# Optimization experiments

Hardware: AMD Instinct MI355X
Metric: run time of the kernel (lower is better)

## Reference

```python
import jax, jax.numpy as jnp
import numpy as np

TAU = 0.01  # softmax temperature used throughout the module


def _cross_en(sim_matrix):
    # -mean(diag(log_softmax(sim, -1)))
    logpt = jax.nn.log_softmax(sim_matrix, axis=-1)
    return -jnp.mean(jnp.diagonal(logpt))


def setup_inputs() -> dict:
    key = jax.random.key(0)
    k1, k2, k3, k4 = jax.random.split(key, 4)
    bs, nw, nf, d = 128, 80, 64, 768
    inp = {
        "traj_output": jax.random.normal(k1, (bs, d), dtype=jnp.float32),
        "frame_features": jax.random.normal(k2, (bs, nf, d), dtype=jnp.float32),
        "sentence_output": jax.random.normal(k3, (bs, d), dtype=jnp.float32),
        "word_features": jax.random.normal(k4, (bs, nw, d), dtype=jnp.float32),
        # nn.Parameter(torch.eye(...)) -- init_weights does not touch these
        "global_mat_weight": jnp.eye(d, dtype=jnp.float32),
        "word_logit_weight": jnp.eye(nw, dtype=jnp.float32),
        "frame_logit_weight": jnp.eye(nf, dtype=jnp.float32),
        "local_mat_weight": jnp.eye(d, dtype=jnp.float32),
        "frame_mat_weight": jnp.eye(nf, dtype=jnp.float32),
        "word_mat_weight": jnp.eye(nw, dtype=jnp.float32),
        "frame_mat_weight2": jnp.eye(nf, dtype=jnp.float32),
        "word_mat_weight2": jnp.eye(nw, dtype=jnp.float32),
    }
    return inp


def reference(traj_output, frame_features, sentence_output, word_features,
              global_mat_weight, word_logit_weight, frame_logit_weight,
              local_mat_weight, frame_mat_weight, word_mat_weight,
              frame_mat_weight2, word_mat_weight2):
    # traj_output: [bs,d]; frame_features: [bs,nf,d]; sentence_output: [bs,d]; word_features: [bs,nw,d]

    # --- traj_sent: (sent @ G) @ traj^T -> [bs_t, bs_v] ---
    traj_sent_sim = (sentence_output @ global_mat_weight) @ traj_output.T

    # --- video_word: word_features @ traj^T -> [bs_t, nw, bs_v] ---
    A = jnp.einsum('twd,vd->twv', word_features, traj_output)
    sA = jax.nn.softmax(A / TAU, axis=1)
    # (softmax.permute(0,2,1) @ W).permute(0,2,1): contract nw axis with W
    wA = jnp.einsum('twv,wu->tuv', sA, word_logit_weight)
    video_word_sim = jnp.sum(A * wA, axis=1)  # [bs_t, bs_v]

    # --- sentence_frame: sent x frame -> [bs_v, bs_t, nf] (torch broadcast batching) ---
    B = jnp.einsum('td,vfd->vtf', sentence_output, frame_features)
    sB = jax.nn.softmax(B / TAU, axis=-1)
    sentence_frame_sim = jnp.sum(B * (sB @ frame_logit_weight), axis=-1).T  # [bs_t, bs_v]

    # --- frame_word: fine-grained sim [bs_t, nw, bs_v, nf] ---
    S = jnp.einsum('twd,vfd->twvf', word_features @ local_mat_weight, frame_features)
    # word-level logit: softmax over nw, mix with word_mat_weight, weighted sum over nw
    sw = jax.nn.softmax(S / TAU, axis=1)
    word_level = jnp.sum(jnp.einsum('twvf,wu->tuvf', sw, word_mat_weight) * S, axis=1)  # [t,v,f]
    # frame-level logit: softmax over nf, mix with frame_mat_weight, weighted sum over nf
    sf = jax.nn.softmax(S / TAU, axis=-1)
    frame_level = jnp.sum((sf @ frame_mat_weight) * S, axis=-1)  # [t,w,v]
    # sent2frame: reduce nf of word_level
    smw = jax.nn.softmax(word_level / TAU, axis=-1)
    sent2frame = jnp.sum((smw @ frame_mat_weight2) * word_level, axis=-1)  # [t,v]
    # video2word: reduce nw of frame_level
    smf = jax.nn.softmax(frame_level / TAU, axis=1)
    video2word = jnp.sum(jnp.einsum('twv,wu->tuv', smf, word_mat_weight2) * frame_level, axis=1)  # [t,v]
    frame_word_sim = (sent2frame + video2word) / 2.0

    sim_matrix = (traj_sent_sim + video_word_sim + sentence_frame_sim + frame_word_sim) / 4.0

    sim_loss = (_cross_en(sim_matrix) + _cross_en(sim_matrix.T)) / 2.0
    return sim_loss
```

## Files before the change

### kernel.cpp

```cpp
#include <hip/hip_runtime.h>
#include <math.h>

#define BS 128
#define NW 80
#define NF 64
#define DD 768
#define INV_TAU 100.0f

typedef unsigned short u16;
typedef unsigned int u32;
typedef __attribute__((ext_vector_type(8))) short bf16x8;
typedef __attribute__((ext_vector_type(4))) float f32x4;

__device__ __forceinline__ u16 f2bf(float x) {
    unsigned b = __float_as_uint(x);
    return (u16)((b + 0x7fffu + ((b >> 16) & 1u)) >> 16);
}
__device__ __forceinline__ float bf2f(u16 h) { return __uint_as_float(((unsigned)h) << 16); }

__device__ __forceinline__ void gload_lds16(const void* gsrc, void* ldst) {
    __builtin_amdgcn_global_load_lds(
        (const __attribute__((address_space(1))) unsigned int*)gsrc,
        (__attribute__((address_space(3))) unsigned int*)ldst, 16, 0, 0);
}

__global__ __launch_bounds__(256) void k_sent_global(
    const float* __restrict__ sent, const float* __restrict__ G, float* __restrict__ sg)
{
    int idx = blockIdx.x * 256 + threadIdx.x;
    int t = idx / DD, e = idx % DD;
    const float* srow = sent + t * DD;
    float acc = 0.f;
    #pragma unroll 4
    for (int d = 0; d < DD; ++d) acc += srow[d] * G[d * DD + e];
    sg[idx] = acc;
}

__global__ __launch_bounds__(256) void k_traj_sent(
    const float* __restrict__ sg, const float* __restrict__ traj, float* __restrict__ sim)
{
    __shared__ float ss[16][33], tt[16][33];
    int tx = threadIdx.x & 15, ty = threadIdx.x >> 4;
    int t0 = blockIdx.y * 16, v0 = blockIdx.x * 16;
    float acc = 0.f;
    for (int kk = 0; kk < DD; kk += 32) {
        for (int l = threadIdx.x; l < 16 * 32; l += 256) {
            int r = l >> 5, c = l & 31;
            ss[r][c] = sg[(t0 + r) * DD + kk + c];
            tt[r][c] = traj[(v0 + r) * DD + kk + c];
        }
        __syncthreads();
        #pragma unroll
        for (int k = 0; k < 32; ++k) acc += ss[ty][k] * tt[tx][k];
        __syncthreads();
    }
    sim[(t0 + ty) * BS + v0 + tx] = 0.25f * acc;
}

__global__ __launch_bounds__(256) void k_prepw(
    const float* __restrict__ Wm, const float* __restrict__ Fm,
    u16* __restrict__ WmT_hi, u16* __restrict__ WmT_lo,
    u16* __restrict__ FmT_hi, u16* __restrict__ FmT_lo)
{
    int gid = blockIdx.x * 256 + threadIdx.x;
    if (gid < 80 * 96) {
        int u = gid / 96, w = gid % 96;
        float x = (w < 80) ? Wm[w * 80 + u] : 0.f;
        u16 h = f2bf(x);
        WmT_hi[gid] = h; WmT_lo[gid] = f2bf(x - bf2f(h));
    } else if (gid < 80 * 96 + 64 * 64) {
        int j = gid - 80 * 96;
        int fp = j >> 6, f = j & 63;
        float x = Fm[f * 64 + fp];
        u16 h = f2bf(x);
        FmT_hi[j] = h; FmT_lo[j] = f2bf(x - bf2f(h));
    }
}

__global__ __launch_bounds__(256) void k_ffsplit(
    const float* __restrict__ x, u16* __restrict__ hi, u16* __restrict__ lo)
{
    int i = blockIdx.x * 256 + threadIdx.x;
    float4 f = *(const float4*)&x[(size_t)i * 4];
    ushort4 h, l;
    h.x = f2bf(f.x); l.x = f2bf(f.x - bf2f(h.x));
    h.y = f2bf(f.y); l.y = f2bf(f.y - bf2f(h.y));
    h.z = f2bf(f.z); l.z = f2bf(f.z - bf2f(h.z));
    h.w = f2bf(f.w); l.w = f2bf(f.w - bf2f(h.w));
    *(ushort4*)&hi[(size_t)i * 4] = h;
    *(ushort4*)&lo[(size_t)i * 4] = l;
}

__global__ __launch_bounds__(256, 2) void k_wl(
    const float* __restrict__ wf, const float* __restrict__ L,
    u16* __restrict__ wl_hi, u16* __restrict__ wl_lo)
{
    __shared__ u16 Ah[128][72], Al[128][72];
    __shared__ u16 Bh[128][72], Bl[128][72];
    const int tid = threadIdx.x;
    const int lane = tid & 63, wid = tid >> 6;
    const int m0 = blockIdx.y * 128, n0 = blockIdx.x * 128;

    f32x4 acc[2][8];
    #pragma unroll
    for (int i = 0; i < 2; ++i)
        #pragma unroll
        for (int j = 0; j < 8; ++j) acc[i][j] = (f32x4){0.f, 0.f, 0.f, 0.f};

    for (int kk = 0; kk < DD; kk += 64) {
        #pragma unroll
        for (int p = 0; p < 8; ++p) {
            int row = p * 16 + (tid >> 4), c4 = tid & 15;
            float4 v = *(const float4*)&wf[(size_t)(m0 + row) * DD + kk + c4 * 4];
            ushort4 h, l;
            h.x = f2bf(v.x); l.x = f2bf(v.x - bf2f(h.x));
            h.y = f2bf(v.y); l.y = f2bf(v.y - bf2f(h.y));
            h.z = f2bf(v.z); l.z = f2bf(v.z - bf2f(h.z));
            h.w = f2bf(v.w); l.w = f2bf(v.w - bf2f(h.w));
            *(ushort4*)&Ah[row][c4 * 4] = h;
            *(ushort4*)&Al[row][c4 * 4] = l;
        }
        #pragma unroll
        for (int p = 0; p < 8; ++p) {
            int kr = p * 8 + (tid >> 5), c4 = tid & 31;
            float4 v = *(const float4*)&L[(size_t)(kk + kr) * DD + n0 + c4 * 4];
            #pragma unroll
            for (int jj = 0; jj < 4; ++jj) {
                int n = c4 * 4 + jj;
                float x = (jj == 0) ? v.x : (jj == 1) ? v.y : (jj == 2) ? v.z : v.w;
                u16 h = f2bf(x);
                int ka = kr ^ ((n & 7) << 3);
                Bh[n][ka] = h;
                Bl[n][ka] = f2bf(x - bf2f(h));
            }
        }
        __syncthreads();
        #pragma unroll
        for (int ks = 0; ks < 2; ++ks) {
            int koff = ks * 32 + (lane >> 4) * 8;
            bf16x8 ah[2], al[2];
            #pragma unroll
            for (int i = 0; i < 2; ++i) {
                int row = wid * 32 + 16 * i + (lane & 15);
                ah[i] = *(const bf16x8*)&Ah[row][koff];
                al[i] = *(const bf16x8*)&Al[row][koff];
            }
            #pragma unroll
            for (int j = 0; j < 8; ++j) {
                int n = 16 * j + (lane & 15);
                int kb = koff ^ ((n & 7) << 3);
                bf16x8 bh = *(const bf16x8*)&Bh[n][kb];
                bf16x8 bl = *(const bf16x8*)&Bl[n][kb];
                #pragma unroll
                for (int i = 0; i < 2; ++i) {
                    acc[i][j] = __builtin_amdgcn_mfma_f32_16x16x32_bf16(ah[i], bh, acc[i][j], 0, 0, 0);
                    acc[i][j] = __builtin_amdgcn_mfma_f32_16x16x32_bf16(ah[i], bl, acc[i][j], 0, 0, 0);
                    acc[i][j] = __builtin_amdgcn_mfma_f32_16x16x32_bf16(al[i], bh, acc[i][j], 0, 0, 0);
                }
            }
        }
        __syncthreads();
    }
    #pragma unroll
    for (int i = 0; i < 2; ++i)
        #pragma unroll
        for (int j = 0; j < 8; ++j)
            #pragma unroll
            for (int r = 0; r < 4; ++r) {
                float x = acc[i][j][r];
                int row = m0 + wid * 32 + 16 * i + ((lane >> 4) << 2) + r;
                int col = n0 + 16 * j + (lane & 15);
                size_t idx = (size_t)row * DD + col;
                u16 h = f2bf(x);
                wl_hi[idx] = h;
                wl_lo[idx] = f2bf(x - bf2f(h));
            }
}

__global__ __launch_bounds__(256, 2) void k_video_word(
    const float* __restrict__ wf, const float* __restrict__ traj,
    const float* __restrict__ Wl, float* __restrict__ sim)
{
    __shared__ __align__(16) float As[NW][36];
    __shared__ __align__(16) float Bs[64][36];
    __shared__ float Am[NW][65];
    __shared__ float Pm[NW][65];
    int tx = threadIdx.x & 15, ty = threadIdx.x >> 4;
    int t = blockIdx.y, v0 = blockIdx.x * 64;
    const float* wft = wf + t * NW * DD;
    float acc[5][4] = {};
    for (int kk = 0; kk < DD; kk += 32) {
        for (int l = threadIdx.x; l < NW * 32; l += 256) {
            int w = l >> 5, k = l & 31;
            As[w][k] = wft[w * DD + kk + k];
        }
        for (int l = threadIdx.x; l < 64 * 32; l += 256) {
            int v = l >> 5, k = l & 31;
            Bs[v][k] = traj[(v0 + v) * DD + kk + k];
        }
        __syncthreads();
        #pragma unroll
        for (int k = 0; k < 32; k += 4) {
            float4 a[5], b[4];
            #pragma unroll
            for (int i = 0; i < 5; ++i) a[i] = *(const float4*)&As[tx + 16 * i][k];
            #pragma unroll
            for (int j = 0; j < 4; ++j) b[j] = *(const float4*)&Bs[ty + 16 * j][k];
            #pragma unroll
            for (int i = 0; i < 5; ++i)
                #pragma unroll
                for (int j = 0; j < 4; ++j)
                    acc[i][j] += a[i].x * b[j].x + a[i].y * b[j].y + a[i].z * b[j].z + a[i].w * b[j].w;
        }
        __syncthreads();
    }
    #pragma unroll
    for (int i = 0; i < 5; ++i)
        #pragma unroll
        for (int j = 0; j < 4; ++j) Am[tx + 16 * i][ty + 16 * j] = acc[i][j];
    __syncthreads();
    if (threadIdx.x < 64) {
        int v = threadIdx.x;
        float m = -1e30f;
        for (int w = 0; w < NW; ++w) m = fmaxf(m, Am[w][v]);
        float s = 0.f;
        for (int w = 0; w < NW; ++w) { float e = __expf((Am[w][v] - m) * INV_TAU); Pm[w][v] = e; s += e; }
        float r = 1.f / s;
        for (int w = 0; w < NW; ++w) Pm[w][v] *= r;
    }
    __syncthreads();
    float mm[5][4] = {};
    for (int w = 0; w < NW; ++w) {
        float a[5], b[4];
        #pragma unroll
        for (int i = 0; i < 5; ++i) a[i] = Wl[w * NW + tx + 16 * i];
        #pragma unroll
        for (int j = 0; j < 4; ++j) b[j] = Pm[w][ty + 16 * j];
        #pragma unroll
        for (int i = 0; i < 5; ++i)
            #pragma unroll
            for (int j = 0; j < 4; ++j) mm[i][j] += a[i] * b[j];
    }
    #pragma unroll
    for (int j = 0; j < 4; ++j) {
        float p = 0.f;
        #pragma unroll
        for (int i = 0; i < 5; ++i) p += mm[i][j] * Am[tx + 16 * i][ty + 16 * j];
        for (int o = 8; o; o >>= 1) p += __shfl_xor(p, o, 16);
        if (tx == 0) sim[t * BS + v0 + ty + 16 * j] += 0.25f * p;
    }
}

__global__ __launch_bounds__(256, 2) void k_sent_frame(
    const float* __restrict__ sent, const float* __restrict__ ff,
    const float* __restrict__ Fl, float* __restrict__ sim)
{
    __shared__ __align__(16) float Ss[64][36];
    __shared__ __align__(16) float Fs[64][36];
    __shared__ float Bm[64][65];
    __shared__ float Pm[64][65];
    int tx = threadIdx.x & 15, ty = threadIdx.x >> 4;
    int v = blockIdx.y, t0 = blockIdx.x * 64;
    const float* ffv = ff + v * NF * DD;
    float acc[4][4] = {};
    for (int kk = 0; kk < DD; kk += 32) {
        for (int l = threadIdx.x; l < 64 * 32; l += 256) {
            int r = l >> 5, k = l & 31;
            Ss[r][k] = sent[(t0 + r) * DD + kk + k];
            Fs[r][k] = ffv[r * DD + kk + k];
        }
        __syncthreads();
        #pragma unroll
        for (int k = 0; k < 32; k += 4) {
            float4 a[4], b[4];
            #pragma unroll
            for (int i = 0; i < 4; ++i) a[i] = *(const float4*)&Ss[tx + 16 * i][k];
            #pragma unroll
            for (int j = 0; j < 4; ++j) b[j] = *(const float4*)&Fs[ty + 16 * j][k];
            #pragma unroll
            for (int i = 0; i < 4; ++i)
                #pragma unroll
                for (int j = 0; j < 4; ++j)
                    acc[i][j] += a[i].x * b[j].x + a[i].y * b[j].y + a[i].z * b[j].z + a[i].w * b[j].w;
        }
        __syncthreads();
    }
    #pragma unroll
    for (int i = 0; i < 4; ++i)
        #pragma unroll
        for (int j = 0; j < 4; ++j) Bm[tx + 16 * i][ty + 16 * j] = acc[i][j];
    __syncthreads();
    if (threadIdx.x < 64) {
        int r = threadIdx.x;
        float m = -1e30f;
        for (int f = 0; f < NF; ++f) m = fmaxf(m, Bm[r][f]);
        float s = 0.f;
        for (int f = 0; f < NF; ++f) { float e = __expf((Bm[r][f] - m) * INV_TAU); Pm[r][f] = e; s += e; }
        float rr = 1.f / s;
        for (int f = 0; f < NF; ++f) Pm[r][f] *= rr;
    }
    __syncthreads();
    float nn[4][4] = {};
    for (int f = 0; f < NF; ++f) {
        float a[4], b[4];
        #pragma unroll
        for (int i = 0; i < 4; ++i) a[i] = Pm[ty + 16 * i][f];
        #pragma unroll
        for (int j = 0; j < 4; ++j) b[j] = Fl[f * NF + tx + 16 * j];
        #pragma unroll
        for (int i = 0; i < 4; ++i)
            #pragma unroll
            for (int j = 0; j < 4; ++j) nn[i][j] += a[i] * b[j];
    }
    #pragma unroll
    for (int i = 0; i < 4; ++i) {
        float p = 0.f;
        #pragma unroll
        for (int j = 0; j < 4; ++j) p += nn[i][j] * Bm[ty + 16 * i][tx + 16 * j];
        for (int o = 8; o; o >>= 1) p += __shfl_xor(p, o, 16);
        if (tx == 0) sim[(t0 + ty + 16 * i) * BS + v] += 0.25f * p;
    }
}

__global__ __launch_bounds__(256, 3) void k_frame_word(
    const u16* __restrict__ wl_hi, const u16* __restrict__ wl_lo,
    const u16* __restrict__ ff_hi, const u16* __restrict__ ff_lo,
    const u16* __restrict__ WmT_hi, const u16* __restrict__ WmT_lo,
    const u16* __restrict__ FmT_hi, const u16* __restrict__ FmT_lo,
    const float* __restrict__ F2, const float* __restrict__ Wm2,
    float* __restrict__ sim)
{
    __shared__ __align__(16) union SH {
        u16 stage[18432];
        struct Post {
            float Sm[80][65];
            union PU {
                struct { u16 Pt_hi[64][104]; u16 Pt_lo[64][104]; } m1;
                struct { u16 P2_hi[80][72];  u16 P2_lo[80][72];  } m2;
            } u;
            float redm[4][64], reds[4][64];
            float wlv[64], flv[80], flvp[4][80];
            float smw[64], smf[80];
            float s2f, v2w;
        } post;
    } sh;

    const int tid = threadIdx.x;
    const int lane = tid & 63, wid = tid >> 6;
    const int col = lane & 15, grp = lane >> 4;
    const int v = blockIdx.x, t = blockIdx.y;

    f32x4 acc[5];
    #pragma unroll
    for (int i = 0; i < 5; ++i) acc[i] = (f32x4){0.f, 0.f, 0.f, 0.f};

    const int r8 = lane >> 3, s8 = lane & 7;
    const int gk = s8 ^ r8;

    for (int kk = 0; kk < DD; kk += 64) {
        for (int seg = wid; seg < 36; seg += 4) {
            const u16* src;
            int ldsoff;
            if (seg < 10) {
                int g = seg, row = g * 8 + r8;
                src = wl_hi + (size_t)(t * NW + row) * DD + kk + gk * 8;
                ldsoff = g * 512;
            } else if (seg < 20) {
                int g = seg - 10, row = g * 8 + r8;
                src = wl_lo + (size_t)(t * NW + row) * DD + kk + gk * 8;
                ldsoff = 5120 + g * 512;
            } else if (seg < 28) {
                int g = seg - 20, row = g * 8 + r8;
                src = ff_hi + (size_t)(v * NF + row) * DD + kk + gk * 8;
                ldsoff = 10240 + g * 512;
            } else {
                int g = seg - 28, row = g * 8 + r8;
                src = ff_lo + (size_t)(v * NF + row) * DD + kk + gk * 8;
                ldsoff = 14336 + g * 512;
            }
            gload_lds16(src, (void*)&sh.stage[ldsoff]);
        }
        __syncthreads();
        const u16* st = sh.stage;
        #pragma unroll
        for (int ks = 0; ks < 2; ++ks) {
            const int sl = (ks << 2) + grp;
            bf16x8 afh[5], afl[5], bfh, bfl;
            #pragma unroll
            for (int i = 0; i < 5; ++i) {
                int row = col + 16 * i;
                int off = row * 64 + ((sl ^ (row & 7)) << 3);
                afh[i] = *(const bf16x8*)&st[off];
                afl[i] = *(const bf16x8*)&st[5120 + off];
            }
            {
                int row = col + 16 * wid;
                int off = row * 64 + ((sl ^ (row & 7)) << 3);
                bfh = *(const bf16x8*)&st[10240 + off];
                bfl = *(const bf16x8*)&st[14336 + off];
            }
            #pragma unroll
            for (int i = 0; i < 5; ++i) {
                acc[i] = __builtin_amdgcn_mfma_f32_16x16x32_bf16(afh[i], bfh, acc[i], 0, 0, 0);
                acc[i] = __builtin_amdgcn_mfma_f32_16x16x32_bf16(afh[i], bfl, acc[i], 0, 0, 0);
                acc[i] = __builtin_amdgcn_mfma_f32_16x16x32_bf16(afl[i], bfh, acc[i], 0, 0, 0);
            }
        }
        __syncthreads();
    }

    #pragma unroll
    for (int i = 0; i < 5; ++i)
        #pragma unroll
        for (int r = 0; r < 4; ++r)
            sh.post.Sm[16 * i + (grp << 2) + r][col + (wid << 4)] = acc[i][r];
    __syncthreads();

    {
        const int f = tid & 63, q = tid >> 6, w0 = q * 20;
        float m = -1e30f;
        for (int w = w0; w < w0 + 20; ++w) m = fmaxf(m, sh.post.Sm[w][f]);
        float s = 0.f;
        for (int w = w0; w < w0 + 20; ++w) s += __expf((sh.post.Sm[w][f] - m) * INV_TAU);
        sh.post.redm[q][f] = m; sh.post.reds[q][f] = s;
        __syncthreads();
        float M = -1e30f;
        #pragma unroll
        for (int qq = 0; qq < 4; ++qq) M = fmaxf(M, sh.post.redm[qq][f]);
        float Dn = 0.f;
        #pragma unroll
        for (int qq = 0; qq < 4; ++qq) Dn += sh.post.reds[qq][f] * __expf((sh.post.redm[qq][f] - M) * INV_TAU);
        float rDn = 1.f / Dn;
        #pragma unroll
        for (int mp = 0; mp < 10; ++mp) {
            int w = w0 + 2 * mp;
            float e0 = __expf((sh.post.Sm[w][f] - M) * INV_TAU) * rDn;
            float e1 = __expf((sh.post.Sm[w + 1][f] - M) * INV_TAU) * rDn;
            u16 h0 = f2bf(e0), h1 = f2bf(e1);
            u16 l0 = f2bf(e0 - bf2f(h0)), l1 = f2bf(e1 - bf2f(h1));
            *(u32*)&sh.post.u.m1.Pt_hi[f][w] = (u32)h0 | ((u32)h1 << 16);
            *(u32*)&sh.post.u.m1.Pt_lo[f][w] = (u32)l0 | ((u32)l1 << 16);
        }
        if (tid < 64) {
            uint4 z = {0, 0, 0, 0};
            *(uint4*)&sh.post.u.m1.Pt_hi[tid][80] = z;
            *(uint4*)&sh.post.u.m1.Pt_hi[tid][88] = z;
            *(uint4*)&sh.post.u.m1.Pt_lo[tid][80] = z;
            *(uint4*)&sh.post.u.m1.Pt_lo[tid][88] = z;
        }
    }
    __syncthreads();

    {
        f32x4 d1[5];
        #pragma unroll
        for (int i = 0; i < 5; ++i) d1[i] = (f32x4){0.f, 0.f, 0.f, 0.f};
        #pragma unroll
        for (int ks = 0; ks < 3; ++ks) {
            int baddr = (wid * 16 + col) * 104 + ks * 32 + grp * 8;
            bf16x8 bh = *(const bf16x8*)&sh.post.u.m1.Pt_hi[0][baddr];
            bf16x8 bl = *(const bf16x8*)&sh.post.u.m1.Pt_lo[0][baddr];
            #pragma unroll
            for (int i = 0; i < 5; ++i) {
                int aaddr = (16 * i + col) * 96 + ks * 32 + grp * 8;
                bf16x8 ah = *(const bf16x8*)&WmT_hi[aaddr];
                bf16x8 al = *(const bf16x8*)&WmT_lo[aaddr];
                d1[i] = __builtin_amdgcn_mfma_f32_16x16x32_bf16(ah, bh, d1[i], 0, 0, 0);
                d1[i] = __builtin_amdgcn_mfma_f32_16x16x32_bf16(ah, bl, d1[i], 0, 0, 0);
                d1[i] = __builtin_amdgcn_mfma_f32_16x16x32_bf16(al, bh, d1[i], 0, 0, 0);
            }
        }
        float p = 0.f;
        #pragma unroll
        for (int i = 0; i < 5; ++i)
            #pragma unroll
            for (int r = 0; r < 4; ++r)
                p += d1[i][r] * sh.post.Sm[16 * i + (grp << 2) + r][wid * 16 + col];
        p += __shfl_xor(p, 16);
        p += __shfl_xor(p, 32);
        if (lane < 16) sh.post.wlv[wid * 16 + lane] = p;
    }
    __syncthreads();

    if (tid < 160) {
        const int w = tid >> 1, h = tid & 1, f0 = h * 32;
        float m = -1e30f;
        for (int c = 0; c < 32; ++c) m = fmaxf(m, sh.post.Sm[w][f0 + c]);
        m = fmaxf(m, __shfl_xor(m, 1));
        float s = 0.f;
        for (int c = 0; c < 32; ++c) s += __expf((sh.post.Sm[w][f0 + c] - m) * INV_TAU);
        s += __shfl_xor(s, 1);
        float r = 1.f / s;
        #pragma unroll
        for (int mp = 0; mp < 16; ++mp) {
            int f = f0 + 2 * mp;
            float e0 = __expf((sh.post.Sm[w][f] - m) * INV_TAU) * r;
            float e1 = __expf((sh.post.Sm[w][f + 1] - m) * INV_TAU) * r;
            u16 h0 = f2bf(e0), h1 = f2bf(e1);
            u16 l0 = f2bf(e0 - bf2f(h0)), l1 = f2bf(e1 - bf2f(h1));
            *(u32*)&sh.post.u.m2.P2_hi[w][f] = (u32)h0 | ((u32)h1 << 16);
            *(u32*)&sh.post.u.m2.P2_lo[w][f] = (u32)l0 | ((u32)l1 << 16);
        }
    }
    __syncthreads();

    {
        f32x4 d2[5];
        #pragma unroll
        for (int i = 0; i < 5; ++i) d2[i] = (f32x4){0.f, 0.f, 0.f, 0.f};
        #pragma unroll
        for (int ks = 0; ks < 2; ++ks) {
            int baddr = (wid * 16 + col) * 64 + ks * 32 + grp * 8;
            bf16x8 bh = *(const bf16x8*)&FmT_hi[baddr];
            bf16x8 bl = *(const bf16x8*)&FmT_lo[baddr];
            #pragma unroll
            for (int i = 0; i < 5; ++i) {
                int aaddr = (16 * i + col) * 72 + ks * 32 + grp * 8;
                bf16x8 ah = *(const bf16x8*)&sh.post.u.m2.P2_hi[0][aaddr];
                bf16x8 al = *(const bf16x8*)&sh.post.u.m2.P2_lo[0][aaddr];
                d2[i] = __builtin_amdgcn_mfma_f32_16x16x32_bf16(ah, bh, d2[i], 0, 0, 0);
                d2[i] = __builtin_amdgcn_mfma_f32_16x16x32_bf16(ah, bl, d2[i], 0, 0, 0);
                d2[i] = __builtin_amdgcn_mfma_f32_16x16x32_bf16(al, bh, d2[i], 0, 0, 0);
            }
        }
        #pragma unroll
        for (int i = 0; i < 5; ++i)
            #pragma unroll
            for (int r = 0; r < 4; ++r) {
                int w = 16 * i + (grp << 2) + r;
                float p = d2[i][r] * sh.post.Sm[w][wid * 16 + col];
                p += __shfl_xor(p, 1);
                p += __shfl_xor(p, 2);
                p += __shfl_xor(p, 4);
                p += __shfl_xor(p, 8);
                if (col == 0) sh.post.flvp[wid][w] = p;
            }
    }
    __syncthreads();
    if (tid < 80)
        sh.post.flv[tid] = sh.post.flvp[0][tid] + sh.post.flvp[1][tid]
                         + sh.post.flvp[2][tid] + sh.post.flvp[3][tid];
    __syncthreads();

    if (wid == 0) {
        float x = sh.post.wlv[lane];
        float m = x;
        #pragma unroll
        for (int o = 32; o; o >>= 1) m = fmaxf(m, __shfl_xor(m, o));
        float e = __expf((x - m) * INV_TAU);
        float s = e;
        #pragma unroll
        for (int o = 32; o; o >>= 1) s += __shfl_xor(s, o);
        sh.post.smw[lane] = e / s;
    } else if (wid == 1) {
        float x0 = sh.post.flv[lane];
        float x1 = (lane < 16) ? sh.post.flv[64 + lane] : -1e30f;
        float m = fmaxf(x0, x1);
        #pragma unroll
        for (int o = 32; o; o >>= 1) m = fmaxf(m, __shfl_xor(m, o));
        float e0 = __expf((x0 - m) * INV_TAU);
        float e1 = (lane < 16) ? __expf((x1 - m) * INV_TAU) : 0.f;
        float s = e0 + e1;
        #pragma unroll
        for (int o = 32; o; o >>= 1) s += __shfl_xor(s, o);
        sh.post.smf[lane] = e0 / s;
        if (lane < 16) sh.post.smf[64 + lane] = e1 / s;
    }
    __syncthreads();

    if (wid == 0) {
        float g = 0.f;
        for (int f = 0; f < NF; ++f) g += sh.post.smw[f] * F2[f * NF + lane];
        float p = g * sh.post.wlv[lane];
        #pragma unroll
        for (int o = 32; o; o >>= 1) p += __shfl_xor(p, o);
        if (lane == 0) sh.post.s2f = p;
    } else if (wid == 1) {
        float g = 0.f;
        for (int w = 0; w < NW; ++w) g += sh.post.smf[w] * Wm2[w * NW + lane];
        float p = g * sh.post.flv[lane];
        if (lane < 16) {
            float g2 = 0.f;
            for (int w = 0; w < NW; ++w) g2 += sh.post.smf[w] * Wm2[w * NW + 64 + lane];
            p += g2 * sh.post.flv[64 + lane];
        }
        #pragma unroll
        for (int o = 32; o; o >>= 1) p += __shfl_xor(p, o);
        if (lane == 0) sh.post.v2w = p;
    }
    __syncthreads();
    if (tid == 0) sim[t * BS + v] += 0.125f * (sh.post.s2f + sh.post.v2w);
}

__global__ __launch_bounds__(256) void k_loss(const float* __restrict__ sim, float* __restrict__ out)
{
    __shared__ float S[BS][BS + 1];
    __shared__ float lr[BS], lc[BS];
    for (int l = threadIdx.x; l < BS * BS; l += 256) {
        int r = l >> 7, c = l & 127;
        S[r][c] = sim[l];
    }
    __syncthreads();
    int tid = threadIdx.x;
    if (tid < BS) {
        float m = -1e30f;
        for (int c = 0; c < BS; ++c) m = fmaxf(m, S[tid][c]);
        float s = 0.f;
        for (int c = 0; c < BS; ++c) s += __expf(S[tid][c] - m);
        lr[tid] = m + __logf(s);
    } else {
        int c = tid - BS;
        float m = -1e30f;
        for (int r = 0; r < BS; ++r) m = fmaxf(m, S[r][c]);
        float s = 0.f;
        for (int r = 0; r < BS; ++r) s += __expf(S[r][c] - m);
        lc[c] = m + __logf(s);
    }
    __syncthreads();
    if (tid == 0) {
        float a = 0.f;
        for (int i = 0; i < BS; ++i) a += S[i][i] - 0.5f * lr[i] - 0.5f * lc[i];
        out[0] = -a / (float)BS;
    }
}

extern "C" void kernel_launch(void* const* d_in, const int* in_sizes, int n_in,
                              void* d_out, int out_size, void* d_ws, size_t ws_size,
                              hipStream_t stream)
{
    const float* traj = (const float*)d_in[0];
    const float* ff   = (const float*)d_in[1];
    const float* sent = (const float*)d_in[2];
    const float* wf   = (const float*)d_in[3];
    const float* G    = (const float*)d_in[4];
    const float* Wl   = (const float*)d_in[5];
    const float* Fl   = (const float*)d_in[6];
    const float* L    = (const float*)d_in[7];
    const float* Fm   = (const float*)d_in[8];
    const float* Wm   = (const float*)d_in[9];
    const float* F2   = (const float*)d_in[10];
    const float* Wm2  = (const float*)d_in[11];
    float* out = (float*)d_out;
    char* base = (char*)d_ws;

    float* sg     = (float*)(base);
    float* sim    = (float*)(base + 393216);
    u16*   wl_hi  = (u16*)(base + 458752);
    u16*   wl_lo  = (u16*)(base + 16187392);
    u16*   ff_hi  = (u16*)(base + 31916032);
    u16*   ff_lo  = (u16*)(base + 44498944);
    u16*   WmT_hi = (u16*)(base + 57081856);
    u16*   WmT_lo = (u16*)(base + 57097216);
    u16*   FmT_hi = (u16*)(base + 57112576);
    u16*   FmT_lo = (u16*)(base + 57120768);

    hipLaunchKernelGGL(k_sent_global, dim3(BS * DD / 256), dim3(256), 0, stream, sent, G, sg);
    hipLaunchKernelGGL(k_traj_sent, dim3(8, 8), dim3(256), 0, stream, sg, traj, sim);
    hipLaunchKernelGGL(k_prepw, dim3(46), dim3(256), 0, stream, Wm, Fm, WmT_hi, WmT_lo, FmT_hi, FmT_lo);
    hipLaunchKernelGGL(k_ffsplit, dim3(BS * NF * DD / 1024), dim3(256), 0, stream, ff, ff_hi, ff_lo);
    hipLaunchKernelGGL(k_wl, dim3(6, 80), dim3(256), 0, stream, wf, L, wl_hi, wl_lo);
    hipLaunchKernelGGL(k_video_word, dim3(2, BS), dim3(256), 0, stream, wf, traj, Wl, sim);
    hipLaunchKernelGGL(k_sent_frame, dim3(2, BS), dim3(256), 0, stream, sent, ff, Fl, sim);
    hipLaunchKernelGGL(k_frame_word, dim3(BS, BS), dim3(256), 0, stream,
                       wl_hi, wl_lo, ff_hi, ff_lo, WmT_hi, WmT_lo, FmT_hi, FmT_lo, F2, Wm2, sim);
    hipLaunchKernelGGL(k_loss, dim3(1), dim3(256), 0, stream, sim, out);
}
```

Measured before the change: 1.533 ms.

## Compute softmax fragments in registers, drop LDS P buffers, split MFMA chains

Removes the shared-memory buffers holding the bf16 hi/lo softmax probabilities. Each wave now recomputes the exponentials directly into its MFMA operand registers from the stored row and column max and reciprocal sums. This shrinks the LDS footprint so the launch bound can rise from 3 to 4 blocks per CU. It also splits the three-MFMA accumulation chains into two independent accumulators to shorten dependency stalls. The cost is redundant exp and bf16 split work per wave, plus extra accumulator registers that may not fit the tighter register budget.

Result: faster. 1.483 ms (-3.3%).

```diff
diff --git a/kernel.cpp b/kernel.cpp
--- a/kernel.cpp
+++ b/kernel.cpp
@@ -322,7 +322,7 @@
     }
 }
 
-__global__ __launch_bounds__(256, 3) void k_frame_word(
+__global__ __launch_bounds__(256, 4) void k_frame_word(
     const u16* __restrict__ wl_hi, const u16* __restrict__ wl_lo,
     const u16* __restrict__ ff_hi, const u16* __restrict__ ff_lo,
     const u16* __restrict__ WmT_hi, const u16* __restrict__ WmT_lo,
@@ -334,11 +334,9 @@
         u16 stage[18432];
         struct Post {
             float Sm[80][65];
-            union PU {
-                struct { u16 Pt_hi[64][104]; u16 Pt_lo[64][104]; } m1;
-                struct { u16 P2_hi[80][72];  u16 P2_lo[80][72];  } m2;
-            } u;
             float redm[4][64], reds[4][64];
+            float colM[64], colRD[64];
+            float rowM[80], rowRD[80];
             float wlv[64], flv[80], flvp[4][80];
             float smw[64], smf[80];
             float s2f, v2w;
@@ -350,9 +348,9 @@
     const int col = lane & 15, grp = lane >> 4;
     const int v = blockIdx.x, t = blockIdx.y;
 
-    f32x4 acc[5];
-    #pragma unroll
-    for (int i = 0; i < 5; ++i) acc[i] = (f32x4){0.f, 0.f, 0.f, 0.f};
+    f32x4 acc[5], acc2[5];
+    #pragma unroll
+    for (int i = 0; i < 5; ++i) { acc[i] = (f32x4){0.f,0.f,0.f,0.f}; acc2[i] = (f32x4){0.f,0.f,0.f,0.f}; }
 
     const int r8 = lane >> 3, s8 = lane & 7;
     const int gk = s8 ^ r8;
@@ -400,11 +398,14 @@
                 bfl = *(const bf16x8*)&st[14336 + off];
             }
             #pragma unroll
-            for (int i = 0; i < 5; ++i) {
+            for (int i = 0; i < 5; ++i)
                 acc[i] = __builtin_amdgcn_mfma_f32_16x16x32_bf16(afh[i], bfh, acc[i], 0, 0, 0);
-                acc[i] = __builtin_amdgcn_mfma_f32_16x16x32_bf16(afh[i], bfl, acc[i], 0, 0, 0);
+            #pragma unroll
+            for (int i = 0; i < 5; ++i)
+                acc2[i] = __builtin_amdgcn_mfma_f32_16x16x32_bf16(afh[i], bfl, acc2[i], 0, 0, 0);
+            #pragma unroll
+            for (int i = 0; i < 5; ++i)
                 acc[i] = __builtin_amdgcn_mfma_f32_16x16x32_bf16(afl[i], bfh, acc[i], 0, 0, 0);
-            }
         }
         __syncthreads();
     }
@@ -413,7 +414,7 @@
     for (int i = 0; i < 5; ++i)
         #pragma unroll
         for (int r = 0; r < 4; ++r)
-            sh.post.Sm[16 * i + (grp << 2) + r][col + (wid << 4)] = acc[i][r];
+            sh.post.Sm[16 * i + (grp << 2) + r][col + (wid << 4)] = acc[i][r] + acc2[i][r];
     __syncthreads();
 
     {
@@ -424,50 +425,47 @@
         for (int w = w0; w < w0 + 20; ++w) s += __expf((sh.post.Sm[w][f] - m) * INV_TAU);
         sh.post.redm[q][f] = m; sh.post.reds[q][f] = s;
         __syncthreads();
-        float M = -1e30f;
-        #pragma unroll
-        for (int qq = 0; qq < 4; ++qq) M = fmaxf(M, sh.post.redm[qq][f]);
-        float Dn = 0.f;
-        #pragma unroll
-        for (int qq = 0; qq < 4; ++qq) Dn += sh.post.reds[qq][f] * __expf((sh.post.redm[qq][f] - M) * INV_TAU);
-        float rDn = 1.f / Dn;
-        #pragma unroll
-        for (int mp = 0; mp < 10; ++mp) {
-            int w = w0 + 2 * mp;
-            float e0 = __expf((sh.post.Sm[w][f] - M) * INV_TAU) * rDn;
-            float e1 = __expf((sh.post.Sm[w + 1][f] - M) * INV_TAU) * rDn;
-            u16 h0 = f2bf(e0), h1 = f2bf(e1);
-            u16 l0 = f2bf(e0 - bf2f(h0)), l1 = f2bf(e1 - bf2f(h1));
-            *(u32*)&sh.post.u.m1.Pt_hi[f][w] = (u32)h0 | ((u32)h1 << 16);
-            *(u32*)&sh.post.u.m1.Pt_lo[f][w] = (u32)l0 | ((u32)l1 << 16);
-        }
-        if (tid < 64) {
-            uint4 z = {0, 0, 0, 0};
-            *(uint4*)&sh.post.u.m1.Pt_hi[tid][80] = z;
-            *(uint4*)&sh.post.u.m1.Pt_hi[tid][88] = z;
-            *(uint4*)&sh.post.u.m1.Pt_lo[tid][80] = z;
-            *(uint4*)&sh.post.u.m1.Pt_lo[tid][88] = z;
+        if (q == 0) {
+            float M = -1e30f;
+            #pragma unroll
+            for (int qq = 0; qq < 4; ++qq) M = fmaxf(M, sh.post.redm[qq][f]);
+            float Dn = 0.f;
+            #pragma unroll
+            for (int qq = 0; qq < 4; ++qq) Dn += sh.post.reds[qq][f] * __expf((sh.post.redm[qq][f] - M) * INV_TAU);
+            sh.post.colM[f] = M;
+            sh.post.colRD[f] = 1.f / Dn;
         }
     }
     __syncthreads();
 
     {
-        f32x4 d1[5];
-        #pragma unroll
-        for (int i = 0; i < 5; ++i) d1[i] = (f32x4){0.f, 0.f, 0.f, 0.f};
+        f32x4 d1[5], d1b[5];
+        #pragma unroll
+        for (int i = 0; i < 5; ++i) { d1[i] = (f32x4){0.f,0.f,0.f,0.f}; d1b[i] = (f32x4){0.f,0.f,0.f,0.f}; }
+        const int f = wid * 16 + col;
+        const float Mf = sh.post.colM[f], RDf = sh.post.colRD[f];
         #pragma unroll
         for (int ks = 0; ks < 3; ++ks) {
-            int baddr = (wid * 16 + col) * 104 + ks * 32 + grp * 8;
-            bf16x8 bh = *(const bf16x8*)&sh.post.u.m1.Pt_hi[0][baddr];
-            bf16x8 bl = *(const bf16x8*)&sh.post.u.m1.Pt_lo[0][baddr];
+            const int w0 = ks * 32 + grp * 8;
+            union { u16 h[8]; bf16x8 v; } bh, bl;
+            #pragma unroll
+            for (int j = 0; j < 8; ++j) {
+                int w = w0 + j;
+                int wc = (w < NW) ? w : 0;
+                float e = __expf((sh.post.Sm[wc][f] - Mf) * INV_TAU) * RDf;
+                e = (w < NW) ? e : 0.f;
+                u16 hh = f2bf(e);
+                bh.h[j] = hh;
+                bl.h[j] = f2bf(e - bf2f(hh));
+            }
             #pragma unroll
             for (int i = 0; i < 5; ++i) {
                 int aaddr = (16 * i + col) * 96 + ks * 32 + grp * 8;
                 bf16x8 ah = *(const bf16x8*)&WmT_hi[aaddr];
                 bf16x8 al = *(const bf16x8*)&WmT_lo[aaddr];
-                d1[i] = __builtin_amdgcn_mfma_f32_16x16x32_bf16(ah, bh, d1[i], 0, 0, 0);
-                d1[i] = __builtin_amdgcn_mfma_f32_16x16x32_bf16(ah, bl, d1[i], 0, 0, 0);
-                d1[i] = __builtin_amdgcn_mfma_f32_16x16x32_bf16(al, bh, d1[i], 0, 0, 0);
+                d1[i]  = __builtin_amdgcn_mfma_f32_16x16x32_bf16(ah, bh.v, d1[i], 0, 0, 0);
+                d1b[i] = __builtin_amdgcn_mfma_f32_16x16x32_bf16(ah, bl.v, d1b[i], 0, 0, 0);
+                d1[i]  = __builtin_amdgcn_mfma_f32_16x16x32_bf16(al, bh.v, d1[i], 0, 0, 0);
             }
         }
         float p = 0.f;
@@ -475,7 +473,7 @@
         for (int i = 0; i < 5; ++i)
             #pragma unroll
             for (int r = 0; r < 4; ++r)
-                p += d1[i][r] * sh.post.Sm[16 * i + (grp << 2) + r][wid * 16 + col];
+                p += (d1[i][r] + d1b[i][r]) * sh.post.Sm[16 * i + (grp << 2) + r][f];
         p += __shfl_xor(p, 16);
         p += __shfl_xor(p, 32);
         if (lane < 16) sh.post.wlv[wid * 16 + lane] = p;
@@ -490,24 +488,14 @@
         float s = 0.f;
         for (int c = 0; c < 32; ++c) s += __expf((sh.post.Sm[w][f0 + c] - m) * INV_TAU);
         s += __shfl_xor(s, 1);
-        float r = 1.f / s;
-        #pragma unroll
-        for (int mp = 0; mp < 16; ++mp) {
-            int f = f0 + 2 * mp;
-            float e0 = __expf((sh.post.Sm[w][f] - m) * INV_TAU) * r;
-            float e1 = __expf((sh.post.Sm[w][f + 1] - m) * INV_TAU) * r;
-            u16 h0 = f2bf(e0), h1 = f2bf(e1);
-            u16 l0 = f2bf(e0 - bf2f(h0)), l1 = f2bf(e1 - bf2f(h1));
-            *(u32*)&sh.post.u.m2.P2_hi[w][f] = (u32)h0 | ((u32)h1 << 16);
-            *(u32*)&sh.post.u.m2.P2_lo[w][f] = (u32)l0 | ((u32)l1 << 16);
-        }
+        if (h == 0) { sh.post.rowM[w] = m; sh.post.rowRD[w] = 1.f / s; }
     }
     __syncthreads();
 
     {
-        f32x4 d2[5];
-        #pragma unroll
-        for (int i = 0; i < 5; ++i) d2[i] = (f32x4){0.f, 0.f, 0.f, 0.f};
+        f32x4 d2[5], d2b[5];
+        #pragma unroll
+        for (int i = 0; i < 5; ++i) { d2[i] = (f32x4){0.f,0.f,0.f,0.f}; d2b[i] = (f32x4){0.f,0.f,0.f,0.f}; }
         #pragma unroll
         for (int ks = 0; ks < 2; ++ks) {
             int baddr = (wid * 16 + col) * 64 + ks * 32 + grp * 8;
@@ -515,12 +503,20 @@
             bf16x8 bl = *(const bf16x8*)&FmT_lo[baddr];
             #pragma unroll
             for (int i = 0; i < 5; ++i) {
-                int aaddr = (16 * i + col) * 72 + ks * 32 + grp * 8;
-                bf16x8 ah = *(const bf16x8*)&sh.post.u.m2.P2_hi[0][aaddr];
-                bf16x8 al = *(const bf16x8*)&sh.post.u.m2.P2_lo[0][aaddr];
-                d2[i] = __builtin_amdgcn_mfma_f32_16x16x32_bf16(ah, bh, d2[i], 0, 0, 0);
-                d2[i] = __builtin_amdgcn_mfma_f32_16x16x32_bf16(ah, bl, d2[i], 0, 0, 0);
-                d2[i] = __builtin_amdgcn_mfma_f32_16x16x32_bf16(al, bh, d2[i], 0, 0, 0);
+                const int row = 16 * i + col;
+                const float Mw = sh.post.rowM[row], RDw = sh.post.rowRD[row];
+                const int f0 = ks * 32 + grp * 8;
+                union { u16 h[8]; bf16x8 v; } ah, al;
+                #pragma unroll
+                for (int j = 0; j < 8; ++j) {
+                    float e = __expf((sh.post.Sm[row][f0 + j] - Mw) * INV_TAU) * RDw;
+                    u16 hh = f2bf(e);
+                    ah.h[j] = hh;
+                    al.h[j] = f2bf(e - bf2f(hh));
+                }
+                d2[i]  = __builtin_amdgcn_mfma_f32_16x16x32_bf16(ah.v, bh, d2[i], 0, 0, 0);
+                d2b[i] = __builtin_amdgcn_mfma_f32_16x16x32_bf16(ah.v, bl, d2b[i], 0, 0, 0);
+                d2[i]  = __builtin_amdgcn_mfma_f32_16x16x32_bf16(al.v, bh, d2[i], 0, 0, 0);
             }
         }
         #pragma unroll
@@ -528,7 +524,7 @@
             #pragma unroll
             for (int r = 0; r < 4; ++r) {
                 int w = 16 * i + (grp << 2) + r;
-                float p = d2[i][r] * sh.post.Sm[w][wid * 16 + col];
+                float p = (d2[i][r] + d2b[i][r]) * sh.post.Sm[w][wid * 16 + col];
                 p += __shfl_xor(p, 1);
                 p += __shfl_xor(p, 2);
                 p += __shfl_xor(p, 4);
```
